# Kernel tuning notes

Hardware: AMD Instinct MI355X
Metric: run time of the kernel (lower is better)

Reference implementation:

```python
import jax, jax.numpy as jnp
import numpy as np
import math

NUM_HEADS = 16
THETA = 10000.0


def _rope(x, token_pos, theta):
    # x: [B, H, S, d_k]; token_pos: [S]
    d_k = x.shape[-1]
    freqs = 1.0 / theta ** (jnp.arange(0, d_k, 2, dtype=jnp.float32) / d_k)  # [d_k/2]
    angles = token_pos.astype(jnp.float32)[:, None] * freqs[None, :]         # [S, d_k/2]
    cos, sin = jnp.cos(angles), jnp.sin(angles)
    x1 = x[..., 0::2]
    x2 = x[..., 1::2]
    out1 = x1 * cos - x2 * sin
    out2 = x1 * sin + x2 * cos
    # interleave back: (..., d_k/2, 2) -> (..., d_k)
    return jnp.stack([out1, out2], axis=-1).reshape(x.shape)


def setup_inputs() -> dict:
    key = jax.random.key(0)
    ks = jax.random.split(key, 5)
    B, S, D = 4, 2048, 1024
    scale = 0.02
    return {
        "x": jax.random.normal(ks[0], (B, S, D), dtype=jnp.float32),
        "token_pos": jnp.arange(S, dtype=jnp.int64 if jax.config.jax_enable_x64 else jnp.int32),
        "Wq": jax.random.normal(ks[1], (D, D), dtype=jnp.float32) * scale,
        "Wk": jax.random.normal(ks[2], (D, D), dtype=jnp.float32) * scale,
        "Wv": jax.random.normal(ks[3], (D, D), dtype=jnp.float32) * scale,
        "Wo": jax.random.normal(ks[4], (D, D), dtype=jnp.float32) * scale,
    }


def reference(x, token_pos, Wq, Wk, Wv, Wo):
    B, S, D = x.shape
    H = NUM_HEADS
    d_k = D // H
    # projections (Linear without bias: y = x @ W^T, W is [out, in])
    def proj(W):
        y = jnp.einsum('bsd,ed->bse', x, W)
        return y.reshape(B, S, H, d_k).transpose(0, 2, 1, 3)  # [B,H,S,d_k]
    q, k, v = proj(Wq), proj(Wk), proj(Wv)
    q = _rope(q, token_pos, THETA)
    k = _rope(k, token_pos, THETA)
    scores = jnp.einsum('bhqd,bhkd->bhqk', q, k) / math.sqrt(d_k)
    causal = jnp.tril(jnp.ones((S, S), dtype=bool))
    scores = jnp.where(causal, scores, -jnp.inf)
    attn = jax.nn.softmax(scores, axis=-1)
    out = jnp.einsum('bhqk,bhkd->bhqd', attn, v)            # [B,H,S,d_k]
    out = out.transpose(0, 2, 1, 3).reshape(B, S, D)
    return jnp.einsum('bsd,ed->bse', out, Wo)
```

## Files before the change

### kernel.cpp

```cpp
#include <hip/hip_runtime.h>

typedef unsigned short u16;
typedef __bf16 bf16x8 __attribute__((ext_vector_type(8)));
typedef float f32x4 __attribute__((ext_vector_type(4)));
typedef u16 u16x8 __attribute__((ext_vector_type(8)));

#define B_ 4
#define S_ 2048
#define D_ 1024
#define H_ 16
#define LOG2E 1.44269504f

__device__ inline u16 f2bf(float f) {
  unsigned u = __float_as_uint(f);
  u = u + 0x7fffu + ((u >> 16) & 1u);
  return (u16)(u >> 16);
}
__device__ inline u16 f2bf_hw(float f) {
  __bf16 b = (__bf16)f;
  return __builtin_bit_cast(u16, b);
}
__device__ inline float bf2f(u16 h) {
  return __uint_as_float(((unsigned)h) << 16);
}
__device__ inline void gload_lds16(const u16* g, u16* l) {
  __builtin_amdgcn_global_load_lds((const __attribute__((address_space(1))) void*)g,
                                   (__attribute__((address_space(3))) void*)l, 16, 0, 0);
}

__global__ __launch_bounds__(256) void k_f32_to_bf16(const float* __restrict__ src,
                                                     u16* __restrict__ dst, int n4) {
  int i = blockIdx.x * 256 + threadIdx.x;
  if (i >= n4) return;
  float4 v = reinterpret_cast<const float4*>(src)[i];
  ushort4 o;
  o.x = f2bf(v.x); o.y = f2bf(v.y); o.z = f2bf(v.z); o.w = f2bf(v.w);
  reinterpret_cast<ushort4*>(dst)[i] = o;
}

__global__ __launch_bounds__(256) void k_cvt_w4(const float* __restrict__ w0,
                                                const float* __restrict__ w1,
                                                const float* __restrict__ w2,
                                                const float* __restrict__ w3,
                                                u16* __restrict__ dst) {
  int i = blockIdx.x * 256 + threadIdx.x;
  const int tensor = i >> 18;
  const int local = i & 262143;
  const float* s = tensor == 0 ? w0 : tensor == 1 ? w1 : tensor == 2 ? w2 : w3;
  float4 v = reinterpret_cast<const float4*>(s)[local];
  ushort4 o;
  o.x = f2bf(v.x); o.y = f2bf(v.y); o.z = f2bf(v.z); o.w = f2bf(v.w);
  reinterpret_cast<ushort4*>(dst + (size_t)tensor * 1048576)[local] = o;
}

__global__ __launch_bounds__(256) void k_rope_table(const int* __restrict__ pos,
                                                    float2* __restrict__ tab) {
  int idx = blockIdx.x * 256 + threadIdx.x;
  if (idx >= S_ * 32) return;
  int s = idx >> 5, i = idx & 31;
  float freq = powf(10000.0f, -(float)i * (1.0f / 32.0f));
  float ang = (float)pos[s] * freq;
  float sn, c;
  sincosf(ang, &sn, &c);
  tab[idx] = make_float2(c, sn);
}

__global__ __launch_bounds__(256) void k_rope_k(u16* __restrict__ kb,
                                                const float2* __restrict__ tab) {
  int idx = blockIdx.x * 256 + threadIdx.x;
  const int row = idx >> 7;
  const int s = row & 2047;
  const int chunk = idx & 127;
  u16* p = kb + ((size_t)row << 10) + chunk * 8;
  u16x8 v = *reinterpret_cast<u16x8*>(p);
  const float4* tp = reinterpret_cast<const float4*>(tab + s * 32 + (chunk & 7) * 4);
  float4 t0 = tp[0], t1 = tp[1];
  float cc[4] = {t0.x, t0.z, t1.x, t1.z};
  float ss[4] = {t0.y, t0.w, t1.y, t1.w};
  u16x8 o;
#pragma unroll
  for (int u = 0; u < 4; u++) {
    float x1 = bf2f(v[2 * u]), x2 = bf2f(v[2 * u + 1]);
    o[2 * u]     = f2bf(x1 * cc[u] - x2 * ss[u]);
    o[2 * u + 1] = f2bf(x1 * ss[u] + x2 * cc[u]);
  }
  *reinterpret_cast<u16x8*>(p) = o;
}

__global__ __launch_bounds__(256) void k_gemm_qkv(const u16* __restrict__ A,
                                                  const u16* __restrict__ Bcat,
                                                  u16* __restrict__ Ccat) {
  __shared__ u16 As[128 * 32];
  __shared__ u16 Bs[128 * 32];
  const int K = 1024;
  const int swz = (blockIdx.x & 7) * 192 + (blockIdx.x >> 3);
  const int bx = swz % 24;
  const int by = swz / 24;
  const int m0 = by << 7, n0 = bx << 7;
  const int tid = threadIdx.x;
  const int lane = tid & 63;
  const int wv = tid >> 6;
  const int wm = (wv >> 1) << 6;
  const int wn = (wv & 1) << 6;
  const int r = lane & 15, g = lane >> 4;

  f32x4 acc[4][4] = {};

  const int o0 = tid << 4;
  const int o1 = o0 + 4096;
  const int am0 = o0 >> 6, ak0 = (o0 & 63) >> 1;
  const int am1 = o1 >> 6, ak1 = (o1 & 63) >> 1;

  for (int k0 = 0; k0 < K; k0 += 32) {
    gload_lds16(A + (size_t)(m0 + am0) * K + k0 + ak0, As + (o0 >> 1));
    gload_lds16(A + (size_t)(m0 + am1) * K + k0 + ak1, As + (o1 >> 1));
    gload_lds16(Bcat + (size_t)(n0 + am0) * K + k0 + ak0, Bs + (o0 >> 1));
    gload_lds16(Bcat + (size_t)(n0 + am1) * K + k0 + ak1, Bs + (o1 >> 1));
    __syncthreads();
    bf16x8 af[4], bfr[4];
#pragma unroll
    for (int i = 0; i < 4; i++)
      af[i] = *reinterpret_cast<const bf16x8*>(&As[(wm + i * 16 + r) * 32 + g * 8]);
#pragma unroll
    for (int t = 0; t < 4; t++)
      bfr[t] = *reinterpret_cast<const bf16x8*>(&Bs[(wn + t * 16 + r) * 32 + g * 8]);
#pragma unroll
    for (int i = 0; i < 4; i++)
#pragma unroll
      for (int t = 0; t < 4; t++)
        acc[i][t] = __builtin_amdgcn_mfma_f32_16x16x32_bf16(af[i], bfr[t], acc[i][t], 0, 0, 0);
    __syncthreads();
  }

  u16* Cb = Ccat + (size_t)(n0 >> 10) * (8192 * 1024);
  const int c0 = n0 & 1023;
#pragma unroll
  for (int i = 0; i < 4; i++) {
#pragma unroll
    for (int t = 0; t < 4; t++) {
      const int row = m0 + wm + i * 16 + g * 4;
      const int col = c0 + wn + t * 16 + r;
#pragma unroll
      for (int j = 0; j < 4; j++)
        Cb[(size_t)(row + j) * 1024 + col] = f2bf(acc[i][t][j]);
    }
  }
}

__global__ __launch_bounds__(256) void k_gemm_bt(const u16* __restrict__ A,
                                                 const u16* __restrict__ Bw,
                                                 float* __restrict__ C,
                                                 int M, int N, int K) {
  __shared__ u16 As[128 * 32];
  __shared__ u16 Bs[128 * 32];
  const int nbx = N >> 7;
  const int swz = (blockIdx.x & 7) * (gridDim.x >> 3) + (blockIdx.x >> 3);
  const int bx = swz % nbx;
  const int by = swz / nbx;
  const int m0 = by << 7, n0 = bx << 7;
  const int tid = threadIdx.x;
  const int lane = tid & 63;
  const int wv = tid >> 6;
  const int wm = (wv >> 1) << 6;
  const int wn = (wv & 1) << 6;
  const int r = lane & 15, g = lane >> 4;

  f32x4 acc[4][4] = {};

  const int o0 = tid << 4;
  const int o1 = o0 + 4096;
  const int am0 = o0 >> 6, ak0 = (o0 & 63) >> 1;
  const int am1 = o1 >> 6, ak1 = (o1 & 63) >> 1;

  for (int k0 = 0; k0 < K; k0 += 32) {
    gload_lds16(A + (size_t)(m0 + am0) * K + k0 + ak0, As + (o0 >> 1));
    gload_lds16(A + (size_t)(m0 + am1) * K + k0 + ak1, As + (o1 >> 1));
    gload_lds16(Bw + (size_t)(n0 + am0) * K + k0 + ak0, Bs + (o0 >> 1));
    gload_lds16(Bw + (size_t)(n0 + am1) * K + k0 + ak1, Bs + (o1 >> 1));
    __syncthreads();
    bf16x8 af[4], bfr[4];
#pragma unroll
    for (int i = 0; i < 4; i++)
      af[i] = *reinterpret_cast<const bf16x8*>(&As[(wm + i * 16 + r) * 32 + g * 8]);
#pragma unroll
    for (int t = 0; t < 4; t++)
      bfr[t] = *reinterpret_cast<const bf16x8*>(&Bs[(wn + t * 16 + r) * 32 + g * 8]);
#pragma unroll
    for (int i = 0; i < 4; i++)
#pragma unroll
      for (int t = 0; t < 4; t++)
        acc[i][t] = __builtin_amdgcn_mfma_f32_16x16x32_bf16(af[i], bfr[t], acc[i][t], 0, 0, 0);
    __syncthreads();
  }

#pragma unroll
  for (int i = 0; i < 4; i++) {
#pragma unroll
    for (int t = 0; t < 4; t++) {
      const int row = m0 + wm + i * 16 + g * 4;
      const int col = n0 + wn + t * 16 + r;
#pragma unroll
      for (int j = 0; j < 4; j++)
        C[(size_t)(row + j) * N + col] = acc[i][t][j];
    }
  }
}

__global__ __launch_bounds__(256) void k_transpose_v(const u16* __restrict__ Vb,
                                                     u16* __restrict__ Vt) {
  __shared__ u16 tile[64][65];
  int bh = blockIdx.x >> 5;
  int st = blockIdx.x & 31;
  int b = bh >> 4, h = bh & 15;
  int s0 = st << 6;
  int tid = threadIdx.x;
#pragma unroll
  for (int rr = 0; rr < 16; rr++) {
    int idx = rr * 256 + tid;
    int sl = idx >> 6, d = idx & 63;
    tile[d][sl] = Vb[(size_t)(b * S_ + s0 + sl) * 1024 + h * 64 + d];
  }
  __syncthreads();
#pragma unroll
  for (int rr = 0; rr < 16; rr++) {
    int idx = rr * 256 + tid;
    int d = idx >> 6, sl = idx & 63;
    Vt[(size_t)(bh * 64 + d) * 2048 + s0 + sl] = tile[d][sl];
  }
}

__global__ __launch_bounds__(256) void k_attn8(const u16* __restrict__ Q,
                                               const u16* __restrict__ Kb,
                                               const u16* __restrict__ Vt,
                                               const float2* __restrict__ tab,
                                               u16* __restrict__ O) {
  __shared__ u16 Ks[2][64 * 64];
  __shared__ u16 Vs[2][64 * 64];
  __shared__ u16 Ps[4][32 * 64];

  const int bh = (blockIdx.x & 7) * 8 + ((blockIdx.x >> 3) & 7);
  const int qt = 15 - (blockIdx.x >> 6);
  const int b = bh >> 4, h = bh & 15;
  const int tid = threadIdx.x;
  const int lane = tid & 63, w = tid >> 6;
  const int g = lane >> 4, r = lane & 15;

  const u16* Kbase = Kb + (size_t)(b * S_) * 1024 + h * 64;
  const u16* Vbase = Vt + (size_t)bh * 64 * 2048;

  const int srow = tid >> 3;
  const int scol = ((tid & 7) * 8) ^ ((srow & 7) * 8);
  const int rsw = (r & 7) * 8;

  const int qbase = qt << 7;
  const int qrow0 = qbase + (w << 5);

  const float QSC = 0.125f * LOG2E;
  bf16x8 qf[2][2];
#pragma unroll
  for (int f = 0; f < 2; f++) {
    const int s = qrow0 + f * 16 + r;
    const u16* qrow = Q + (size_t)(b * S_ + s) * 1024 + h * 64;
    qf[f][0] = *reinterpret_cast<const bf16x8*>(qrow + g * 8);
    qf[f][1] = *reinterpret_cast<const bf16x8*>(qrow + 32 + g * 8);
    const float4* tp = reinterpret_cast<const float4*>(tab + s * 32);
#pragma unroll
    for (int c = 0; c < 2; c++) {
      float4 t0 = tp[c * 8 + g * 2], t1 = tp[c * 8 + g * 2 + 1];
      float cc[4] = {t0.x, t0.z, t1.x, t1.z};
      float ss[4] = {t0.y, t0.w, t1.y, t1.w};
      bf16x8 q = qf[f][c];
#pragma unroll
      for (int u = 0; u < 4; u++) {
        float x1 = (float)q[2 * u], x2 = (float)q[2 * u + 1];
        q[2 * u]     = (__bf16)((x1 * cc[u] - x2 * ss[u]) * QSC);
        q[2 * u + 1] = (__bf16)((x1 * ss[u] + x2 * cc[u]) * QSC);
      }
      qf[f][c] = q;
    }
  }

  f32x4 o_acc[2][4] = {};
  float l0 = 0.f, l1 = 0.f;
  u16* pb0 = &Ps[w][r * 64];
  u16* pb1 = &Ps[w][(16 + r) * 64];

#define STAGE_KV(k0v, bufi)                                                        \
  do {                                                                             \
    gload_lds16(Kbase + (size_t)((k0v) + srow) * 1024 + scol, &Ks[bufi][0] + tid * 8);        \
    gload_lds16(Kbase + (size_t)((k0v) + srow + 32) * 1024 + scol, &Ks[bufi][0] + tid * 8 + 2048); \
    gload_lds16(Vbase + (size_t)srow * 2048 + (k0v) + scol, &Vs[bufi][0] + tid * 8);          \
    gload_lds16(Vbase + (size_t)(srow + 32) * 2048 + (k0v) + scol, &Vs[bufi][0] + tid * 8 + 2048); \
  } while (0)

  const int kend = qbase + 128;

  STAGE_KV(0, 0);
  asm volatile("s_waitcnt vmcnt(0)" ::: "memory");
  __builtin_amdgcn_s_barrier();

  int cur = 0;
  for (int k0 = 0; k0 < kend; k0 += 64) {
    if (k0 + 64 < kend) STAGE_KV(k0 + 64, cur ^ 1);

    if (k0 <= qrow0 + 31) {
      const u16* ks = &Ks[cur][0];
      const u16* vs = &Vs[cur][0];
      const int rem0 = qrow0 + 15 - k0;
      const int rem1 = qrow0 + 31 - k0;
      const int ktlim0 = rem0 < 0 ? 0 : (rem0 >= 48 ? 4 : (rem0 >> 4) + 1);
      const int ktlim1 = rem1 >= 48 ? 4 : (rem1 >> 4) + 1;
      const bool mask0 = (k0 + 63 > qrow0);
      const bool mask1 = (k0 + 63 > qrow0 + 16);

#pragma unroll
      for (int kt = 0; kt < 4; kt++) {
        const int pc = (kt * 16 + g * 4) ^ rsw;
        if (kt >= ktlim1) {
          ushort4 z = {0, 0, 0, 0};
          *reinterpret_cast<ushort4*>(pb0 + pc) = z;
          *reinterpret_cast<ushort4*>(pb1 + pc) = z;
          continue;
        }
        const int krow = kt * 16 + r;
        bf16x8 kf0 = *reinterpret_cast<const bf16x8*>(&ks[krow * 64 + ((g * 8) ^ rsw)]);
        bf16x8 kf1 = *reinterpret_cast<const bf16x8*>(&ks[krow * 64 + ((32 + g * 8) ^ rsw)]);
        f32x4 s0 = {}, s1 = {};
        if (kt < ktlim0) {
          s0 = __builtin_amdgcn_mfma_f32_16x16x32_bf16(kf0, qf[0][0], s0, 0, 0, 0);
          s0 = __builtin_amdgcn_mfma_f32_16x16x32_bf16(kf1, qf[0][1], s0, 0, 0, 0);
        }
        s1 = __builtin_amdgcn_mfma_f32_16x16x32_bf16(kf0, qf[1][0], s1, 0, 0, 0);
        s1 = __builtin_amdgcn_mfma_f32_16x16x32_bf16(kf1, qf[1][1], s1, 0, 0, 0);

        const int colb = k0 + kt * 16 + g * 4;
        float p0[4], p1[4];
        if (kt < ktlim0) {
          if (mask0) {
#pragma unroll
            for (int j = 0; j < 4; j++)
              if (colb + j > qrow0 + r) s0[j] = -1e30f;
          }
#pragma unroll
          for (int j = 0; j < 4; j++) p0[j] = exp2f(s0[j]);
          l0 += (p0[0] + p0[1]) + (p0[2] + p0[3]);
        } else {
#pragma unroll
          for (int j = 0; j < 4; j++) p0[j] = 0.f;
        }
        if (mask1) {
#pragma unroll
          for (int j = 0; j < 4; j++)
            if (colb + j > qrow0 + 16 + r) s1[j] = -1e30f;
        }
#pragma unroll
        for (int j = 0; j < 4; j++) p1[j] = exp2f(s1[j]);
        l1 += (p1[0] + p1[1]) + (p1[2] + p1[3]);

        ushort4 w0, w1;
        w0.x = f2bf_hw(p0[0]); w0.y = f2bf_hw(p0[1]); w0.z = f2bf_hw(p0[2]); w0.w = f2bf_hw(p0[3]);
        w1.x = f2bf_hw(p1[0]); w1.y = f2bf_hw(p1[1]); w1.z = f2bf_hw(p1[2]); w1.w = f2bf_hw(p1[3]);
        *reinterpret_cast<ushort4*>(pb0 + pc) = w0;
        *reinterpret_cast<ushort4*>(pb1 + pc) = w1;
      }
      asm volatile("s_waitcnt lgkmcnt(0)" ::: "memory");

#pragma unroll
      for (int kc = 0; kc < 2; kc++) {
        const int cb = (kc * 32 + g * 8) ^ rsw;
        bf16x8 pf0 = *reinterpret_cast<const bf16x8*>(pb0 + cb);
        bf16x8 pf1 = *reinterpret_cast<const bf16x8*>(pb1 + cb);
#pragma unroll
        for (int dt = 0; dt < 4; dt++) {
          bf16x8 vf = *reinterpret_cast<const bf16x8*>(
              &vs[(dt * 16 + r) * 64 + ((kc * 32 + g * 8) ^ rsw)]);
          o_acc[0][dt] = __builtin_amdgcn_mfma_f32_16x16x32_bf16(pf0, vf, o_acc[0][dt], 0, 0, 0);
          o_acc[1][dt] = __builtin_amdgcn_mfma_f32_16x16x32_bf16(pf1, vf, o_acc[1][dt], 0, 0, 0);
        }
      }
    }

    asm volatile("s_waitcnt vmcnt(0)" ::: "memory");
    __builtin_amdgcn_s_barrier();
    cur ^= 1;
  }
#undef STAGE_KV

  l0 += __shfl_xor(l0, 16); l0 += __shfl_xor(l0, 32);
  l1 += __shfl_xor(l1, 16); l1 += __shfl_xor(l1, 32);

#pragma unroll
  for (int f = 0; f < 2; f++) {
    u16* orow = O + (size_t)(b * S_ + qrow0 + f * 16) * 1024 + h * 64;
#pragma unroll
    for (int j = 0; j < 4; j++) {
      const float ln = __shfl(f ? l1 : l0, 4 * g + j);
      const float rln = 1.0f / ln;
#pragma unroll
      for (int dt = 0; dt < 4; dt++)
        orow[(size_t)(g * 4 + j) * 1024 + dt * 16 + r] = f2bf(o_acc[f][dt][j] * rln);
    }
  }
}

extern "C" void kernel_launch(void* const* d_in, const int* in_sizes, int n_in,
                              void* d_out, int out_size, void* d_ws, size_t ws_size,
                              hipStream_t stream) {
  const float* x  = (const float*)d_in[0];
  const int*   pos = (const int*)d_in[1];
  const float* Wq = (const float*)d_in[2];
  const float* Wk = (const float*)d_in[3];
  const float* Wv = (const float*)d_in[4];
  const float* Wo = (const float*)d_in[5];
  float* out = (float*)d_out;

  char* ws = (char*)d_ws;
  size_t off = 0;
  auto alloc = [&](size_t bytes) {
    void* p = ws + off;
    off += (bytes + 255) & ~(size_t)255;
    return p;
  };
  const size_t XB = (size_t)8192 * 1024 * 2;
  u16* xb  = (u16*)alloc(XB);
  u16* wqb = (u16*)alloc((size_t)1024 * 1024 * 2);
  u16* wkb = (u16*)alloc((size_t)1024 * 1024 * 2);
  u16* wvb = (u16*)alloc((size_t)1024 * 1024 * 2);
  u16* wob = (u16*)alloc((size_t)1024 * 1024 * 2);
  u16* qb  = (u16*)alloc(XB);
  u16* kb  = (u16*)alloc(XB);
  u16* vb  = (u16*)alloc(XB);
  u16* vt  = (u16*)alloc(XB);
  float2* tab = (float2*)alloc((size_t)2048 * 32 * sizeof(float2));
  u16* ob = vb;
  (void)wkb; (void)wvb;

  k_f32_to_bf16<<<8192, 256, 0, stream>>>(x, xb, 2097152);
  k_cvt_w4<<<4096, 256, 0, stream>>>(Wq, Wk, Wv, Wo, wqb);
  k_rope_table<<<256, 256, 0, stream>>>(pos, tab);

  k_gemm_qkv<<<1536, 256, 0, stream>>>(xb, wqb, qb);

  k_rope_k<<<4096, 256, 0, stream>>>(kb, tab);

  k_transpose_v<<<2048, 256, 0, stream>>>(vb, vt);

  k_attn8<<<1024, 256, 0, stream>>>(qb, kb, vt, tab, ob);

  k_gemm_bt<<<512, 256, 0, stream>>>(ob, wob, out, 8192, 1024, 1024);
}
```

Baseline: 203.7 us.

## Single-buffer K/V tiles in attention and raise wave priority around MFMAs

The attention kernel drops double buffering of the K and V shared-memory tiles. It now loads each tile synchronously into a single buffer, with a __syncthreads before and after compute. This cuts LDS use per block from about 48KB to 32KB, so more blocks can be resident per CU and overlap across blocks can replace overlap within a block. It also wraps the QK and PV MFMA sequences in s_setprio so matrix work is favoured when waves compete. The cost is that load latency inside each block is no longer hidden by prefetch.

```diff
diff --git a/kernel.cpp b/kernel.cpp
--- a/kernel.cpp
+++ b/kernel.cpp
@@ -229,13 +229,13 @@
   }
 }
 
-__global__ __launch_bounds__(256) void k_attn8(const u16* __restrict__ Q,
+__global__ __launch_bounds__(256) void k_attn9(const u16* __restrict__ Q,
                                                const u16* __restrict__ Kb,
                                                const u16* __restrict__ Vt,
                                                const float2* __restrict__ tab,
                                                u16* __restrict__ O) {
-  __shared__ u16 Ks[2][64 * 64];
-  __shared__ u16 Vs[2][64 * 64];
+  __shared__ u16 Ks[64 * 64];
+  __shared__ u16 Vs[64 * 64];
   __shared__ u16 Ps[4][32 * 64];
 
   const int bh = (blockIdx.x & 7) * 8 + ((blockIdx.x >> 3) & 7);
@@ -285,27 +285,15 @@
   u16* pb0 = &Ps[w][r * 64];
   u16* pb1 = &Ps[w][(16 + r) * 64];
 
-#define STAGE_KV(k0v, bufi)                                                        \
-  do {                                                                             \
-    gload_lds16(Kbase + (size_t)((k0v) + srow) * 1024 + scol, &Ks[bufi][0] + tid * 8);        \
-    gload_lds16(Kbase + (size_t)((k0v) + srow + 32) * 1024 + scol, &Ks[bufi][0] + tid * 8 + 2048); \
-    gload_lds16(Vbase + (size_t)srow * 2048 + (k0v) + scol, &Vs[bufi][0] + tid * 8);          \
-    gload_lds16(Vbase + (size_t)(srow + 32) * 2048 + (k0v) + scol, &Vs[bufi][0] + tid * 8 + 2048); \
-  } while (0)
-
   const int kend = qbase + 128;
-
-  STAGE_KV(0, 0);
-  asm volatile("s_waitcnt vmcnt(0)" ::: "memory");
-  __builtin_amdgcn_s_barrier();
-
-  int cur = 0;
   for (int k0 = 0; k0 < kend; k0 += 64) {
-    if (k0 + 64 < kend) STAGE_KV(k0 + 64, cur ^ 1);
+    gload_lds16(Kbase + (size_t)(k0 + srow) * 1024 + scol, Ks + tid * 8);
+    gload_lds16(Kbase + (size_t)(k0 + srow + 32) * 1024 + scol, Ks + tid * 8 + 2048);
+    gload_lds16(Vbase + (size_t)srow * 2048 + k0 + scol, Vs + tid * 8);
+    gload_lds16(Vbase + (size_t)(srow + 32) * 2048 + k0 + scol, Vs + tid * 8 + 2048);
+    __syncthreads();
 
     if (k0 <= qrow0 + 31) {
-      const u16* ks = &Ks[cur][0];
-      const u16* vs = &Vs[cur][0];
       const int rem0 = qrow0 + 15 - k0;
       const int rem1 = qrow0 + 31 - k0;
       const int ktlim0 = rem0 < 0 ? 0 : (rem0 >= 48 ? 4 : (rem0 >> 4) + 1);
@@ -323,15 +311,17 @@
           continue;
         }
         const int krow = kt * 16 + r;
-        bf16x8 kf0 = *reinterpret_cast<const bf16x8*>(&ks[krow * 64 + ((g * 8) ^ rsw)]);
-        bf16x8 kf1 = *reinterpret_cast<const bf16x8*>(&ks[krow * 64 + ((32 + g * 8) ^ rsw)]);
+        bf16x8 kf0 = *reinterpret_cast<const bf16x8*>(&Ks[krow * 64 + ((g * 8) ^ rsw)]);
+        bf16x8 kf1 = *reinterpret_cast<const bf16x8*>(&Ks[krow * 64 + ((32 + g * 8) ^ rsw)]);
         f32x4 s0 = {}, s1 = {};
+        __builtin_amdgcn_s_setprio(1);
         if (kt < ktlim0) {
           s0 = __builtin_amdgcn_mfma_f32_16x16x32_bf16(kf0, qf[0][0], s0, 0, 0, 0);
           s0 = __builtin_amdgcn_mfma_f32_16x16x32_bf16(kf1, qf[0][1], s0, 0, 0, 0);
         }
         s1 = __builtin_amdgcn_mfma_f32_16x16x32_bf16(kf0, qf[1][0], s1, 0, 0, 0);
         s1 = __builtin_amdgcn_mfma_f32_16x16x32_bf16(kf1, qf[1][1], s1, 0, 0, 0);
+        __builtin_amdgcn_s_setprio(0);
 
         const int colb = k0 + kt * 16 + g * 4;
         float p0[4], p1[4];
@@ -365,6 +355,7 @@
       }
       asm volatile("s_waitcnt lgkmcnt(0)" ::: "memory");
 
+      __builtin_amdgcn_s_setprio(1);
 #pragma unroll
       for (int kc = 0; kc < 2; kc++) {
         const int cb = (kc * 32 + g * 8) ^ rsw;
@@ -373,18 +364,15 @@
 #pragma unroll
         for (int dt = 0; dt < 4; dt++) {
           bf16x8 vf = *reinterpret_cast<const bf16x8*>(
-              &vs[(dt * 16 + r) * 64 + ((kc * 32 + g * 8) ^ rsw)]);
+              &Vs[(dt * 16 + r) * 64 + ((kc * 32 + g * 8) ^ rsw)]);
           o_acc[0][dt] = __builtin_amdgcn_mfma_f32_16x16x32_bf16(pf0, vf, o_acc[0][dt], 0, 0, 0);
           o_acc[1][dt] = __builtin_amdgcn_mfma_f32_16x16x32_bf16(pf1, vf, o_acc[1][dt], 0, 0, 0);
         }
       }
+      __builtin_amdgcn_s_setprio(0);
     }
-
-    asm volatile("s_waitcnt vmcnt(0)" ::: "memory");
-    __builtin_amdgcn_s_barrier();
-    cur ^= 1;
-  }
-#undef STAGE_KV
+    __syncthreads();
+  }
 
   l0 += __shfl_xor(l0, 16); l0 += __shfl_xor(l0, 32);
   l1 += __shfl_xor(l1, 16); l1 += __shfl_xor(l1, 32);
@@ -445,7 +433,7 @@
 
   k_transpose_v<<<2048, 256, 0, stream>>>(vb, vt);
 
-  k_attn8<<<1024, 256, 0, stream>>>(qb, kb, vt, tab, ob);
+  k_attn9<<<1024, 256, 0, stream>>>(qb, kb, vt, tab, ob);
 
   k_gemm_bt<<<512, 256, 0, stream>>>(ob, wob, out, 8192, 1024, 1024);
 }
```

Measured after the change: 204.0 us. About the same (+0.2%).
